# Performance work log

Hardware: AMD Instinct MI355X
Metric: run time of the kernel (lower is better)

Reference implementation:

```python
import jax, jax.numpy as jnp
import numpy as np

B, T, H = 64, 256, 128

def setup_inputs() -> dict:
    key = jax.random.key(0)
    ks = jax.random.split(key, 10)
    s = 1.0 / np.sqrt(H)
    return {
        "x": jax.random.normal(ks[0], (B, T, 2), jnp.float32),
        "enc_output": jax.random.normal(ks[1], (B, T, H), jnp.float32),
        "h0": jax.random.normal(ks[2], (B, H), jnp.float32) * s,
        "c0": jax.random.normal(ks[3], (B, H), jnp.float32) * s,
        "W1": jax.random.normal(ks[4], (H, H), jnp.float32) * s,
        "W2": jax.random.normal(ks[5], (H, H), jnp.float32) * s,
        "V": jax.random.normal(ks[6], (H,), jnp.float32) * s,
        "Wk": jax.random.normal(ks[7], (2, 4 * H), jnp.float32) * (1.0 / np.sqrt(2.0)),
        "Wr": jax.random.normal(ks[8], (H, 4 * H), jnp.float32) * s,
        "b": jnp.zeros((4 * H,), jnp.float32),
    }


def reference(x, enc_output, h0, c0, W1, W2, V, Wk, Wr, b):
    Bb, Tt, _ = x.shape
    # Precompute W1 @ enc_output once (original recomputes it T times inside K.rnn)
    enc_proj = jnp.einsum('bth,hk->btk', enc_output, W1)  # [B,T,H]

    def lstm_cell(inp, h, c):
        # Keras LSTMCell, gate order i,f,c,o; sigmoid recurrent activation, tanh activation
        z = inp @ Wk + h @ Wr + b  # [B,4H]
        zi, zf, zg, zo = jnp.split(z, 4, axis=-1)
        i = jax.nn.sigmoid(zi)
        f = jax.nn.sigmoid(zf)
        g = jnp.tanh(zg)
        o = jax.nn.sigmoid(zo)
        c_new = f * c + i * g
        h_new = o * jnp.tanh(c_new)
        return h_new, c_new

    def step(carry, _):
        h, c, ptr = carry
        h, c = lstm_cell(ptr, h, c)
        # additive attention over all encoder steps, batched (replaces inner K.rnn)
        scores = jnp.einsum('btk,k->bt', jnp.tanh(enc_proj + (h @ W2)[:, None, :]), V)
        probs = jax.nn.softmax(scores, axis=1)  # [B,T]
        # get_pointer with rank=0: top-1 of descending argsort == argmax
        idx = jnp.argmax(probs, axis=1)  # [B]
        ptr = jnp.take_along_axis(x, idx[:, None, None], axis=1)[:, 0, :]  # [B,2]
        return (h, c, ptr), probs

    ptr0 = jnp.ones((Bb, 2), x.dtype)
    _, probs_seq = jax.lax.scan(step, (h0, c0, ptr0), None, length=Tt)  # [T,B,T]
    return jnp.transpose(probs_seq, (1, 0, 2))  # [B,T,T]
```

## Files before the change

### kernel.cpp

```cpp
#include <hip/hip_runtime.h>
#include <cstddef>

#define TT 256
#define HH 128
#define EST 132
#define SCPS 260

__device__ __forceinline__ float rdlane(float v, int l) {
  return __int_as_float(__builtin_amdgcn_readlane(__float_as_int(v), l));
}
__device__ __forceinline__ float fast_sigmoid(float x) {
  const float L2E = 1.4426950408889634f;
  float y = __builtin_amdgcn_exp2f(-x * L2E);
  return __builtin_amdgcn_rcpf(1.0f + y);
}
__device__ __forceinline__ float fast_tanh(float x) {
  const float C2 = 2.8853900817779268f;
  float y = __builtin_amdgcn_exp2f(x * C2);
  return 1.0f - 2.0f * __builtin_amdgcn_rcpf(1.0f + y);
}

__global__ __attribute__((amdgpu_flat_work_group_size(1024, 1024),
                          amdgpu_waves_per_eu(4, 4)))
void decoder_kernel(const float* __restrict__ x,
                    const float* __restrict__ enc_output,
                    const float* __restrict__ h0,
                    const float* __restrict__ c0,
                    const float* __restrict__ W1,
                    const float* __restrict__ W2,
                    const float* __restrict__ V,
                    const float* __restrict__ Wk,
                    const float* __restrict__ Wr,
                    const float* __restrict__ bias,
                    float* __restrict__ out)
{
  __shared__ float E[TT * EST];
  __shared__ float zpart[4 * 512];
  __shared__ float scp[16 * SCPS];
  __shared__ float hbuf[HH];
  __shared__ float xlds[2 * TT];

  const int u    = threadIdx.x;
  const int b    = blockIdx.x;
  const int lane = u & 63;
  const int w    = u >> 6;
  const float C2  = 2.8853900817779268f;
  const float L2E = 1.4426950408889634f;

  {
    const float* encb = enc_output + (size_t)b * TT * HH;
    const int tsub = u >> 4;
    const int ks   = (u & 15) * 8;
    for (int p = 0; p < 4; ++p) {
      const int tt = p * 64 + tsub;
      float4 a0 = {0.f, 0.f, 0.f, 0.f};
      float4 a1 = {0.f, 0.f, 0.f, 0.f};
      const float4* er4 = (const float4*)(encb + tt * HH);
      for (int j4 = 0; j4 < 32; ++j4) {
        const float4 ev = er4[j4];
        const float* w1p = W1 + (j4 * 4) * HH + ks;
        float4 wa, wb;
        wa = *(const float4*)(w1p + 0 * HH); wb = *(const float4*)(w1p + 0 * HH + 4);
        a0.x += ev.x * wa.x; a0.y += ev.x * wa.y; a0.z += ev.x * wa.z; a0.w += ev.x * wa.w;
        a1.x += ev.x * wb.x; a1.y += ev.x * wb.y; a1.z += ev.x * wb.z; a1.w += ev.x * wb.w;
        wa = *(const float4*)(w1p + 1 * HH); wb = *(const float4*)(w1p + 1 * HH + 4);
        a0.x += ev.y * wa.x; a0.y += ev.y * wa.y; a0.z += ev.y * wa.z; a0.w += ev.y * wa.w;
        a1.x += ev.y * wb.x; a1.y += ev.y * wb.y; a1.z += ev.y * wb.z; a1.w += ev.y * wb.w;
        wa = *(const float4*)(w1p + 2 * HH); wb = *(const float4*)(w1p + 2 * HH + 4);
        a0.x += ev.z * wa.x; a0.y += ev.z * wa.y; a0.z += ev.z * wa.z; a0.w += ev.z * wa.w;
        a1.x += ev.z * wb.x; a1.y += ev.z * wb.y; a1.z += ev.z * wb.z; a1.w += ev.z * wb.w;
        wa = *(const float4*)(w1p + 3 * HH); wb = *(const float4*)(w1p + 3 * HH + 4);
        a0.x += ev.w * wa.x; a0.y += ev.w * wa.y; a0.z += ev.w * wa.z; a0.w += ev.w * wa.w;
        a1.x += ev.w * wb.x; a1.y += ev.w * wb.y; a1.z += ev.w * wb.z; a1.w += ev.w * wb.w;
      }
      *(float4*)(&E[tt * EST + ks])     = a0;
      *(float4*)(&E[tt * EST + ks + 4]) = a1;
    }
    if (u < 2 * TT) xlds[u] = x[b * (TT * 2) + u];
  }

  const int kq  = u >> 8;
  const int cs2 = u & 255;
  float2 wr2[32];
  #pragma unroll
  for (int i = 0; i < 32; ++i)
    wr2[i] = *(const float2*)(Wr + (size_t)(32 * kq + i) * 512 + 2 * cs2);
  const int m = 32 * (w & 3) + (lane & 31);
  float wkA[4], wkB[4], bbg[4];
  #pragma unroll
  for (int gg = 0; gg < 4; ++gg) {
    wkA[gg] = Wk[gg * HH + m];
    wkB[gg] = Wk[512 + gg * HH + m];
    bbg[gg] = bias[gg * HH + m];
  }
  float c = c0[b * HH + m];
  const int kk8 = lane & 7;
  const int jq8 = lane >> 3;
  float w2loc[16];
  #pragma unroll
  for (int i = 0; i < 16; ++i)
    w2loc[i] = W2[(16 * jq8 + i) * HH + 8 * w + kk8];
  const float v2r = -2.0f * V[8 * w + kk8];
  float vL[8];
  #pragma unroll
  for (int i = 0; i < 8; ++i) vL[i] = rdlane(v2r, i);
  float ptr0 = 1.0f, ptr1 = 1.0f;
  float svr;
  {
    float v = V[lane] + V[64 + lane];
    #pragma unroll
    for (int o = 1; o < 64; o <<= 1) v += __shfl_xor(v, o, 64);
    svr = v;
  }

  __syncthreads();

  {
    float* Er = &E[(u >> 2) * EST + 32 * (u & 3)];
    #pragma unroll
    for (int i = 0; i < 8; ++i) {
      float4 ev = *(const float4*)(Er + 4 * i);
      ev.x = __builtin_amdgcn_exp2f(ev.x * C2);
      ev.y = __builtin_amdgcn_exp2f(ev.y * C2);
      ev.z = __builtin_amdgcn_exp2f(ev.z * C2);
      ev.w = __builtin_amdgcn_exp2f(ev.w * C2);
      *(float4*)(Er + 4 * i) = ev;
    }
  }
  {
    float hA0 = h0[(size_t)b * HH + 32 * kq + (lane & 31)];
    float2 zac = {0.f, 0.f};
    #pragma unroll
    for (int i = 0; i < 32; ++i) {
      float hi = rdlane(hA0, i);
      zac.x += hi * wr2[i].x;
      zac.y += hi * wr2[i].y;
    }
    *(float2*)(&zpart[kq * 512 + 2 * cs2]) = zac;
  }
  __syncthreads();

  float* outb = out + (size_t)b * TT * TT;

  #pragma unroll 1
  for (int step = 0; step < TT; ++step) {
    if (step > 0) {
      if (w < 4) {
        float4 sc = {0.f, 0.f, 0.f, 0.f};
        #pragma unroll
        for (int q = 0; q < 16; ++q) {
          const float4 v = *(const float4*)(&scp[q * SCPS + 4 * lane]);
          sc.x += v.x; sc.y += v.y; sc.z += v.z; sc.w += v.w;
        }
        float m4 = fmaxf(fmaxf(sc.x, sc.y), fmaxf(sc.z, sc.w));
        int ttl = (sc.x == m4) ? 0 : (sc.y == m4) ? 1 : (sc.z == m4) ? 2 : 3;
        float mx = m4;
        #pragma unroll
        for (int o = 1; o < 64; o <<= 1) mx = fmaxf(mx, __shfl_xor(mx, o));
        unsigned long long bal = __ballot(m4 == mx);
        int ls  = __ffsll(bal) - 1;
        int tc  = 4 * lane + ttl;
        int tts = __builtin_amdgcn_readlane(tc, ls);
        const float2 pp = *(const float2*)(&xlds[2 * tts]);
        ptr0 = pp.x;
        ptr1 = pp.y;
      } else if (w < 8) {
        float4 sc = {0.f, 0.f, 0.f, 0.f};
        #pragma unroll
        for (int q = 0; q < 16; ++q) {
          const float4 v = *(const float4*)(&scp[q * SCPS + 4 * lane]);
          sc.x += v.x; sc.y += v.y; sc.z += v.z; sc.w += v.w;
        }
        sc.x += svr; sc.y += svr; sc.z += svr; sc.w += svr;
        float p0 = __builtin_amdgcn_exp2f((sc.x - 12.0f) * L2E);
        float p1 = __builtin_amdgcn_exp2f((sc.y - 12.0f) * L2E);
        float p2 = __builtin_amdgcn_exp2f((sc.z - 12.0f) * L2E);
        float p3 = __builtin_amdgcn_exp2f((sc.w - 12.0f) * L2E);
        float ws4 = (p0 + p1) + (p2 + p3);
        #pragma unroll
        for (int o = 1; o < 64; o <<= 1) ws4 += __shfl_xor(ws4, o);
        if ((lane >> 4) == (w - 4)) {
          float rs = __builtin_amdgcn_rcpf(ws4);
          float4 po = {p0 * rs, p1 * rs, p2 * rs, p3 * rs};
          *(float4*)(&outb[(size_t)(step - 1) * TT + 4 * lane]) = po;
        }
      }
    }
    if ((lane & 32) == 0 && w < 4) {
      float z0 = bbg[0] + ptr0 * wkA[0] + ptr1 * wkB[0];
      float z1 = bbg[1] + ptr0 * wkA[1] + ptr1 * wkB[1];
      float z2 = bbg[2] + ptr0 * wkA[2] + ptr1 * wkB[2];
      float z3 = bbg[3] + ptr0 * wkA[3] + ptr1 * wkB[3];
      #pragma unroll
      for (int q = 0; q < 4; ++q) {
        z0 += zpart[q * 512 + 0 * HH + m];
        z1 += zpart[q * 512 + 1 * HH + m];
        z2 += zpart[q * 512 + 2 * HH + m];
        z3 += zpart[q * 512 + 3 * HH + m];
      }
      float ig = fast_sigmoid(z0);
      float fg = fast_sigmoid(z1);
      float gg = fast_tanh(z2);
      float og = fast_sigmoid(z3);
      c = fg * c + ig * gg;
      hbuf[m] = og * fast_tanh(c);
    }
    __syncthreads();

    float Uk;
    {
      float cp0 = 0.0f, cp1 = 0.0f;
      const float4* h4 = (const float4*)(hbuf + 16 * jq8);
      #pragma unroll
      for (int i4 = 0; i4 < 4; ++i4) {
        float4 hv = h4[i4];
        cp0 += hv.x * w2loc[4 * i4 + 0];
        cp1 += hv.y * w2loc[4 * i4 + 1];
        cp0 += hv.z * w2loc[4 * i4 + 2];
        cp1 += hv.w * w2loc[4 * i4 + 3];
      }
      float csum = cp0 + cp1;
      csum += __shfl_xor(csum, 8);
      csum += __shfl_xor(csum, 16);
      csum += __shfl_xor(csum, 32);
      Uk = __builtin_amdgcn_exp2f(csum * C2);
    }
    {
      float uL[8];
      #pragma unroll
      for (int i = 0; i < 8; ++i) uL[i] = rdlane(Uk, i);
      #pragma unroll
      for (int tt = 0; tt < 4; ++tt) {
        const float* Er = &E[(64 * tt + lane) * EST + 8 * w];
        float4 e0 = *(const float4*)(Er + 0);
        float4 e1 = *(const float4*)(Er + 4);
        float a0 = 0.0f, a1 = 0.0f;
        float t0, t1, n;
        t0 = fmaf(e0.x, uL[0], 1.0f); t1 = fmaf(e0.y, uL[1], 1.0f);
        n  = fmaf(vL[1], t0, vL[0] * t1);
        a0 = fmaf(n, __builtin_amdgcn_rcpf(t0 * t1), a0);
        t0 = fmaf(e0.z, uL[2], 1.0f); t1 = fmaf(e0.w, uL[3], 1.0f);
        n  = fmaf(vL[3], t0, vL[2] * t1);
        a1 = fmaf(n, __builtin_amdgcn_rcpf(t0 * t1), a1);
        t0 = fmaf(e1.x, uL[4], 1.0f); t1 = fmaf(e1.y, uL[5], 1.0f);
        n  = fmaf(vL[5], t0, vL[4] * t1);
        a0 = fmaf(n, __builtin_amdgcn_rcpf(t0 * t1), a0);
        t0 = fmaf(e1.z, uL[6], 1.0f); t1 = fmaf(e1.w, uL[7], 1.0f);
        n  = fmaf(vL[7], t0, vL[6] * t1);
        a1 = fmaf(n, __builtin_amdgcn_rcpf(t0 * t1), a1);
        scp[w * SCPS + 64 * tt + lane] = a0 + a1;
      }
    }
    {
      const float4* h4 = (const float4*)(hbuf + 32 * kq);
      float2 zac = {0.f, 0.f};
      #pragma unroll
      for (int i4 = 0; i4 < 8; ++i4) {
        float4 hv = h4[i4];
        zac.x += hv.x * wr2[4 * i4 + 0].x; zac.y += hv.x * wr2[4 * i4 + 0].y;
        zac.x += hv.y * wr2[4 * i4 + 1].x; zac.y += hv.y * wr2[4 * i4 + 1].y;
        zac.x += hv.z * wr2[4 * i4 + 2].x; zac.y += hv.z * wr2[4 * i4 + 2].y;
        zac.x += hv.w * wr2[4 * i4 + 3].x; zac.y += hv.w * wr2[4 * i4 + 3].y;
      }
      *(float2*)(&zpart[kq * 512 + 2 * cs2]) = zac;
    }
    __syncthreads();
  }

  if (w >= 4 && w < 8) {
    float4 sc = {0.f, 0.f, 0.f, 0.f};
    #pragma unroll
    for (int q = 0; q < 16; ++q) {
      const float4 v = *(const float4*)(&scp[q * SCPS + 4 * lane]);
      sc.x += v.x; sc.y += v.y; sc.z += v.z; sc.w += v.w;
    }
    sc.x += svr; sc.y += svr; sc.z += svr; sc.w += svr;
    float p0 = __builtin_amdgcn_exp2f((sc.x - 12.0f) * L2E);
    float p1 = __builtin_amdgcn_exp2f((sc.y - 12.0f) * L2E);
    float p2 = __builtin_amdgcn_exp2f((sc.z - 12.0f) * L2E);
    float p3 = __builtin_amdgcn_exp2f((sc.w - 12.0f) * L2E);
    float ws4 = (p0 + p1) + (p2 + p3);
    #pragma unroll
    for (int o = 1; o < 64; o <<= 1) ws4 += __shfl_xor(ws4, o);
    if ((lane >> 4) == (w - 4)) {
      float rs = __builtin_amdgcn_rcpf(ws4);
      float4 po = {p0 * rs, p1 * rs, p2 * rs, p3 * rs};
      *(float4*)(&outb[(size_t)255 * TT + 4 * lane]) = po;
    }
  }
}

extern "C" void kernel_launch(void* const* d_in, const int* in_sizes, int n_in,
                              void* d_out, int out_size, void* d_ws, size_t ws_size,
                              hipStream_t stream) {
  (void)in_sizes; (void)n_in; (void)d_ws; (void)ws_size; (void)out_size;
  const float* x    = (const float*)d_in[0];
  const float* enc  = (const float*)d_in[1];
  const float* h0   = (const float*)d_in[2];
  const float* c0   = (const float*)d_in[3];
  const float* W1   = (const float*)d_in[4];
  const float* W2   = (const float*)d_in[5];
  const float* V    = (const float*)d_in[6];
  const float* Wk   = (const float*)d_in[7];
  const float* Wr   = (const float*)d_in[8];
  const float* bias = (const float*)d_in[9];
  float* out = (float*)d_out;

  decoder_kernel<<<64, 1024, 0, stream>>>(x, enc, h0, c0, W1, W2, V, Wk, Wr, bias, out);
}
```

Measured before the change: 891.3 us.

## Stream Wr from cache per step, use DPP reductions, reorder recurrent matvec

Drops the 32-entry float2 register cache of Wr and reloads the slices from global memory every step in two halves, prefetched around the barrier, to cut register pressure. Wave reductions now use DPP moves instead of shuffle chains. The W2 mapping is changed so its reduction needs one fewer cross-lane step. The Wr matvec moves ahead of the attention scoring, and a single wave writes the softmax output instead of four. The trade-off is extra global or L2 load traffic on every step of the serial loop.

```diff
diff --git a/kernel.cpp b/kernel.cpp
--- a/kernel.cpp
+++ b/kernel.cpp
@@ -8,6 +8,29 @@
 
 __device__ __forceinline__ float rdlane(float v, int l) {
   return __int_as_float(__builtin_amdgcn_readlane(__float_as_int(v), l));
+}
+template<int CTRL>
+__device__ __forceinline__ float dpp_mv(float x) {
+  return __int_as_float(
+      __builtin_amdgcn_mov_dpp(__float_as_int(x), CTRL, 0xF, 0xF, true));
+}
+__device__ __forceinline__ float wave_max64(float x) {
+  x = fmaxf(x, dpp_mv<0xB1>(x));
+  x = fmaxf(x, dpp_mv<0x4E>(x));
+  x = fmaxf(x, dpp_mv<0x124>(x));
+  x = fmaxf(x, dpp_mv<0x128>(x));
+  x = fmaxf(x, __shfl_xor(x, 16));
+  x = fmaxf(x, __shfl_xor(x, 32));
+  return x;
+}
+__device__ __forceinline__ float wave_sum64(float x) {
+  x += dpp_mv<0xB1>(x);
+  x += dpp_mv<0x4E>(x);
+  x += dpp_mv<0x124>(x);
+  x += dpp_mv<0x128>(x);
+  x += __shfl_xor(x, 16);
+  x += __shfl_xor(x, 32);
+  return x;
 }
 __device__ __forceinline__ float fast_sigmoid(float x) {
   const float L2E = 1.4426950408889634f;
@@ -81,10 +104,7 @@
 
   const int kq  = u >> 8;
   const int cs2 = u & 255;
-  float2 wr2[32];
-  #pragma unroll
-  for (int i = 0; i < 32; ++i)
-    wr2[i] = *(const float2*)(Wr + (size_t)(32 * kq + i) * 512 + 2 * cs2);
+  const float* wrp = Wr + (size_t)(32 * kq) * 512 + 2 * cs2;
   const int m = 32 * (w & 3) + (lane & 31);
   float wkA[4], wkB[4], bbg[4];
   #pragma unroll
@@ -94,23 +114,20 @@
     bbg[gg] = bias[gg * HH + m];
   }
   float c = c0[b * HH + m];
-  const int kk8 = lane & 7;
-  const int jq8 = lane >> 3;
+  const int kk = lane & 7;
+  const int jq = lane >> 3;
   float w2loc[16];
   #pragma unroll
-  for (int i = 0; i < 16; ++i)
-    w2loc[i] = W2[(16 * jq8 + i) * HH + 8 * w + kk8];
-  const float v2r = -2.0f * V[8 * w + kk8];
-  float vL[8];
-  #pragma unroll
-  for (int i = 0; i < 8; ++i) vL[i] = rdlane(v2r, i);
+  for (int ii = 0; ii < 4; ++ii)
+    #pragma unroll
+    for (int cc = 0; cc < 4; ++cc)
+      w2loc[4 * ii + cc] = W2[(4 * jq + 32 * ii + cc) * HH + 8 * w + kk];
+  const float v2r = -2.0f * V[8 * w + kk];
   float ptr0 = 1.0f, ptr1 = 1.0f;
   float svr;
   {
     float v = V[lane] + V[64 + lane];
-    #pragma unroll
-    for (int o = 1; o < 64; o <<= 1) v += __shfl_xor(v, o, 64);
-    svr = v;
+    svr = wave_sum64(v);
   }
 
   __syncthreads();
@@ -132,9 +149,10 @@
     float2 zac = {0.f, 0.f};
     #pragma unroll
     for (int i = 0; i < 32; ++i) {
+      float2 wv = *(const float2*)(wrp + (size_t)i * 512);
       float hi = rdlane(hA0, i);
-      zac.x += hi * wr2[i].x;
-      zac.y += hi * wr2[i].y;
+      zac.x += hi * wv.x;
+      zac.y += hi * wv.y;
     }
     *(float2*)(&zpart[kq * 512 + 2 * cs2]) = zac;
   }
@@ -144,6 +162,11 @@
 
   #pragma unroll 1
   for (int step = 0; step < TT; ++step) {
+    float2 wstA[16];
+    #pragma unroll
+    for (int i = 0; i < 16; ++i)
+      wstA[i] = *(const float2*)(wrp + (size_t)i * 512);
+
     if (step > 0) {
       if (w < 4) {
         float4 sc = {0.f, 0.f, 0.f, 0.f};
@@ -154,9 +177,7 @@
         }
         float m4 = fmaxf(fmaxf(sc.x, sc.y), fmaxf(sc.z, sc.w));
         int ttl = (sc.x == m4) ? 0 : (sc.y == m4) ? 1 : (sc.z == m4) ? 2 : 3;
-        float mx = m4;
-        #pragma unroll
-        for (int o = 1; o < 64; o <<= 1) mx = fmaxf(mx, __shfl_xor(mx, o));
+        float mx = wave_max64(m4);
         unsigned long long bal = __ballot(m4 == mx);
         int ls  = __ffsll(bal) - 1;
         int tc  = 4 * lane + ttl;
@@ -164,7 +185,7 @@
         const float2 pp = *(const float2*)(&xlds[2 * tts]);
         ptr0 = pp.x;
         ptr1 = pp.y;
-      } else if (w < 8) {
+      } else if (w == 4) {
         float4 sc = {0.f, 0.f, 0.f, 0.f};
         #pragma unroll
         for (int q = 0; q < 16; ++q) {
@@ -176,14 +197,10 @@
         float p1 = __builtin_amdgcn_exp2f((sc.y - 12.0f) * L2E);
         float p2 = __builtin_amdgcn_exp2f((sc.z - 12.0f) * L2E);
         float p3 = __builtin_amdgcn_exp2f((sc.w - 12.0f) * L2E);
-        float ws4 = (p0 + p1) + (p2 + p3);
-        #pragma unroll
-        for (int o = 1; o < 64; o <<= 1) ws4 += __shfl_xor(ws4, o);
-        if ((lane >> 4) == (w - 4)) {
-          float rs = __builtin_amdgcn_rcpf(ws4);
-          float4 po = {p0 * rs, p1 * rs, p2 * rs, p3 * rs};
-          *(float4*)(&outb[(size_t)(step - 1) * TT + 4 * lane]) = po;
-        }
+        float ws4 = wave_sum64((p0 + p1) + (p2 + p3));
+        float rs = __builtin_amdgcn_rcpf(ws4);
+        float4 po = {p0 * rs, p1 * rs, p2 * rs, p3 * rs};
+        *(float4*)(&outb[(size_t)(step - 1) * TT + 4 * lane]) = po;
       }
     }
     if ((lane & 32) == 0 && w < 4) {
@@ -207,28 +224,51 @@
     }
     __syncthreads();
 
+    float2 wstB[16];
+    #pragma unroll
+    for (int i = 0; i < 16; ++i)
+      wstB[i] = *(const float2*)(wrp + (size_t)(16 + i) * 512);
+
     float Uk;
     {
-      float cp0 = 0.0f, cp1 = 0.0f;
-      const float4* h4 = (const float4*)(hbuf + 16 * jq8);
-      #pragma unroll
-      for (int i4 = 0; i4 < 4; ++i4) {
-        float4 hv = h4[i4];
-        cp0 += hv.x * w2loc[4 * i4 + 0];
-        cp1 += hv.y * w2loc[4 * i4 + 1];
-        cp0 += hv.z * w2loc[4 * i4 + 2];
-        cp1 += hv.w * w2loc[4 * i4 + 3];
-      }
-      float csum = cp0 + cp1;
-      csum += __shfl_xor(csum, 8);
+      float cp = 0.0f;
+      #pragma unroll
+      for (int ii = 0; ii < 4; ++ii) {
+        const float4 hv = *(const float4*)(hbuf + 4 * jq + 32 * ii);
+        cp += hv.x * w2loc[4 * ii + 0];
+        cp += hv.y * w2loc[4 * ii + 1];
+        cp += hv.z * w2loc[4 * ii + 2];
+        cp += hv.w * w2loc[4 * ii + 3];
+      }
+      float csum = cp;
+      csum += dpp_mv<0x128>(csum);
       csum += __shfl_xor(csum, 16);
       csum += __shfl_xor(csum, 32);
       Uk = __builtin_amdgcn_exp2f(csum * C2);
     }
     {
-      float uL[8];
+      float hv1 = hbuf[32 * kq + (lane & 31)];
+      float2 zac = {0.f, 0.f};
+      #pragma unroll
+      for (int i = 0; i < 16; ++i) {
+        float hi = rdlane(hv1, i);
+        zac.x += hi * wstA[i].x;
+        zac.y += hi * wstA[i].y;
+      }
+      #pragma unroll
+      for (int i = 0; i < 16; ++i) {
+        float hi = rdlane(hv1, 16 + i);
+        zac.x += hi * wstB[i].x;
+        zac.y += hi * wstB[i].y;
+      }
+      *(float2*)(&zpart[kq * 512 + 2 * cs2]) = zac;
+    }
+    {
+      float uL[8], vL[8];
       #pragma unroll
       for (int i = 0; i < 8; ++i) uL[i] = rdlane(Uk, i);
+      #pragma unroll
+      for (int i = 0; i < 8; ++i) vL[i] = rdlane(v2r, i);
       #pragma unroll
       for (int tt = 0; tt < 4; ++tt) {
         const float* Er = &E[(64 * tt + lane) * EST + 8 * w];
@@ -251,23 +291,10 @@
         scp[w * SCPS + 64 * tt + lane] = a0 + a1;
       }
     }
-    {
-      const float4* h4 = (const float4*)(hbuf + 32 * kq);
-      float2 zac = {0.f, 0.f};
-      #pragma unroll
-      for (int i4 = 0; i4 < 8; ++i4) {
-        float4 hv = h4[i4];
-        zac.x += hv.x * wr2[4 * i4 + 0].x; zac.y += hv.x * wr2[4 * i4 + 0].y;
-        zac.x += hv.y * wr2[4 * i4 + 1].x; zac.y += hv.y * wr2[4 * i4 + 1].y;
-        zac.x += hv.z * wr2[4 * i4 + 2].x; zac.y += hv.z * wr2[4 * i4 + 2].y;
-        zac.x += hv.w * wr2[4 * i4 + 3].x; zac.y += hv.w * wr2[4 * i4 + 3].y;
-      }
-      *(float2*)(&zpart[kq * 512 + 2 * cs2]) = zac;
-    }
     __syncthreads();
   }
 
-  if (w >= 4 && w < 8) {
+  if (w == 4) {
     float4 sc = {0.f, 0.f, 0.f, 0.f};
     #pragma unroll
     for (int q = 0; q < 16; ++q) {
@@ -279,14 +306,10 @@
     float p1 = __builtin_amdgcn_exp2f((sc.y - 12.0f) * L2E);
     float p2 = __builtin_amdgcn_exp2f((sc.z - 12.0f) * L2E);
     float p3 = __builtin_amdgcn_exp2f((sc.w - 12.0f) * L2E);
-    float ws4 = (p0 + p1) + (p2 + p3);
-    #pragma unroll
-    for (int o = 1; o < 64; o <<= 1) ws4 += __shfl_xor(ws4, o);
-    if ((lane >> 4) == (w - 4)) {
-      float rs = __builtin_amdgcn_rcpf(ws4);
-      float4 po = {p0 * rs, p1 * rs, p2 * rs, p3 * rs};
-      *(float4*)(&outb[(size_t)255 * TT + 4 * lane]) = po;
-    }
+    float ws4 = wave_sum64((p0 + p1) + (p2 + p3));
+    float rs = __builtin_amdgcn_rcpf(ws4);
+    float4 po = {p0 * rs, p1 * rs, p2 * rs, p3 * rs};
+    *(float4*)(&outb[(size_t)255 * TT + 4 * lane]) = po;
   }
 }
 
```

New measurement: 910.0 us. 1.02x slower.
